# Performance work log

Hardware: AMD Instinct MI355X
Metric: run time of the kernel (lower is better)

The kernel has to match this reference:

```python
import jax, jax.numpy as jnp
import numpy as np
import math

B, QL, HID = 4, 4, 4096          # batch, speculative q_len, hidden_size
NH, NKV, HD = 32, 8, 128         # attention heads, kv heads, head_dim
GROUPS = NH // NKV               # GQA repeat factor = 4
PRIOR = 4096                     # cached (prior) KV length
THETA = 1.0e6                    # Mixtral rope_theta


def setup_inputs() -> dict:
    key = jax.random.key(0)
    ks = jax.random.split(key, 7)
    hidden_states = jax.random.normal(ks[0], (B, QL, HID), jnp.float32)
    past_k = jax.random.normal(ks[1], (B, NKV, PRIOR, HD), jnp.float32)
    past_v = jax.random.normal(ks[2], (B, NKV, PRIOR, HD), jnp.float32)
    wq = jax.random.normal(ks[3], (HID, NH * HD), jnp.float32) * 0.02
    wk = jax.random.normal(ks[4], (HID, NKV * HD), jnp.float32) * 0.02
    wv = jax.random.normal(ks[5], (HID, NKV * HD), jnp.float32) * 0.02
    wo = jax.random.normal(ks[6], (NH * HD, HID), jnp.float32) * 0.02
    # prior mask: all cached positions visible
    attention_mask = jnp.ones((B, 1, QL, PRIOR), dtype=bool)
    # active mask: causal over the speculative window
    active_mask = jnp.broadcast_to(jnp.tril(jnp.ones((QL, QL), dtype=bool)), (B, 1, QL, QL))
    position_ids = jnp.broadcast_to(PRIOR + jnp.arange(QL, dtype=jnp.int64), (B, QL))
    return {"hidden_states": hidden_states, "past_k": past_k, "past_v": past_v,
            "wq": wq, "wk": wk, "wv": wv, "wo": wo,
            "attention_mask": attention_mask, "active_mask": active_mask,
            "position_ids": position_ids}


def _rotate_half(x):
    x1, x2 = jnp.split(x, 2, axis=-1)
    return jnp.concatenate([-x2, x1], axis=-1)


def _rope_cos_sin(position_ids):
    inv_freq = 1.0 / (THETA ** (jnp.arange(0, HD, 2, dtype=jnp.float32) / HD))  # [HD/2]
    freqs = position_ids.astype(jnp.float32)[..., None] * inv_freq              # [B,QL,HD/2]
    emb = jnp.concatenate([freqs, freqs], axis=-1)                              # [B,QL,HD]
    return jnp.cos(emb)[:, None], jnp.sin(emb)[:, None]                          # [B,1,QL,HD]


def reference(hidden_states, past_k, past_v, wq, wk, wv, wo,
              attention_mask, active_mask, position_ids):
    # fused QKV projection (no bias in Mixtral)
    q = (hidden_states @ wq).reshape(B, QL, NH, HD).transpose(0, 2, 1, 3)   # [B,NH,QL,HD]
    k = (hidden_states @ wk).reshape(B, QL, NKV, HD).transpose(0, 2, 1, 3)  # [B,NKV,QL,HD]
    v = (hidden_states @ wv).reshape(B, QL, NKV, HD).transpose(0, 2, 1, 3)
    # RoPE on Q and active K
    cos, sin = _rope_cos_sin(position_ids)
    q = q * cos + _rotate_half(q) * sin
    k = k * cos + _rotate_half(k) * sin
    # GQA repeat_kv
    k_prior = jnp.repeat(past_k, GROUPS, axis=1)  # [B,NH,PRIOR,HD]
    v_prior = jnp.repeat(past_v, GROUPS, axis=1)
    k_active = jnp.repeat(k, GROUPS, axis=1)      # [B,NH,QL,HD]
    v_active = jnp.repeat(v, GROUPS, axis=1)
    scale = 1.0 / math.sqrt(HD)
    neg = jnp.finfo(jnp.float32).min
    prior_scores = jnp.einsum('bhqd,bhkd->bhqk', q, k_prior) * scale
    prior_scores = jnp.where(attention_mask, prior_scores, neg)
    active_scores = jnp.einsum('bhqd,bhkd->bhqk', q, k_active) * scale
    active_scores = jnp.where(active_mask, active_scores, neg)   # is_speculation=True
    # decomposed softmax: shared max and shared divisor across prior/active
    max_score = jnp.maximum(prior_scores.max(-1, keepdims=True),
                            active_scores.max(-1, keepdims=True))
    prior_exp = jnp.exp(prior_scores - max_score)
    active_exp = jnp.exp(active_scores - max_score)
    divisor = prior_exp.sum(-1, keepdims=True) + active_exp.sum(-1, keepdims=True)
    attn = (jnp.einsum('bhqk,bhkd->bhqd', prior_exp / divisor, v_prior) +
            jnp.einsum('bhqk,bhkd->bhqd', active_exp / divisor, v_active))
    attn = attn.transpose(0, 2, 1, 3).reshape(B, QL, NH * HD)
    return attn @ wo
```

## Files before the change

kernel.cpp:

```cpp
#include <hip/hip_runtime.h>
#include <math.h>

#define NROWS 16
#define NCOLS 6144
#define HID   4096
#define NKV   8
#define HD    128
#define PRIOR 4096
#define NCH   32
#define CHUNK 128
#define SUB   64
#define KC1   128
#define NKC   32

__device__ __forceinline__ float rdlane(float v, int l) {
    return __int_as_float(__builtin_amdgcn_readlane(__float_as_int(v), l));
}

__global__ __launch_bounds__(128)
void k_qkv_partial(const float* __restrict__ hid,
                   const float* __restrict__ wq,
                   const float* __restrict__ wk,
                   const float* __restrict__ wv,
                   float* __restrict__ part)
{
    const int t   = threadIdx.x;
    const int col = blockIdx.x * 256 + t * 2;
    const int kc  = blockIdx.y;
    const int k0  = kc * KC1;
    const float* w; int wn, wcol;
    if (col < 4096)      { w = wq; wn = 4096; wcol = col; }
    else if (col < 5120) { w = wk; wn = 1024; wcol = col - 4096; }
    else                 { w = wv; wn = 1024; wcol = col - 5120; }
    const float* wp = w + wcol + (size_t)k0 * wn;

    float acc[NROWS][2];
#pragma unroll
    for (int m = 0; m < NROWS; m++) { acc[m][0] = 0.f; acc[m][1] = 0.f; }
#pragma unroll 4
    for (int kk = 0; kk < KC1; kk += 4) {
        const float2 w0 = *(const float2*)(wp + (size_t)(kk + 0) * wn);
        const float2 w1 = *(const float2*)(wp + (size_t)(kk + 1) * wn);
        const float2 w2 = *(const float2*)(wp + (size_t)(kk + 2) * wn);
        const float2 w3 = *(const float2*)(wp + (size_t)(kk + 3) * wn);
#pragma unroll
        for (int m = 0; m < NROWS; m++) {
            const float4 h4 = *(const float4*)(hid + (size_t)m * HID + k0 + kk);
            acc[m][0] = fmaf(h4.x, w0.x, fmaf(h4.y, w1.x, fmaf(h4.z, w2.x, fmaf(h4.w, w3.x, acc[m][0]))));
            acc[m][1] = fmaf(h4.x, w0.y, fmaf(h4.y, w1.y, fmaf(h4.z, w2.y, fmaf(h4.w, w3.y, acc[m][1]))));
        }
    }
    float* po = part + (size_t)kc * (NROWS * NCOLS) + col;
#pragma unroll
    for (int m = 0; m < NROWS; m++)
        *(float2*)(po + (size_t)m * NCOLS) = make_float2(acc[m][0], acc[m][1]);
}

__global__ __launch_bounds__(256)
void k_reduce_rope(const float* __restrict__ part, float* __restrict__ qkv)
{
    const int tid = blockIdx.x * 256 + threadIdx.x;
    const double L64 = 0.21586735246819178;

    if (tid < 32768) {
        const int d = tid & 63, h = (tid >> 6) & 31, r = tid >> 11;
        const int c1 = h * HD + d;
        float s1 = 0.f, s2 = 0.f;
#pragma unroll 8
        for (int c = 0; c < NKC; c++) {
            const float* p = part + (size_t)c * (NROWS * NCOLS) + r * NCOLS + c1;
            s1 += p[0]; s2 += p[64];
        }
        const double ang = (double)(PRIOR + (r & 3)) * exp(-(double)d * L64);
        double sv, cv; sincos(ang, &sv, &cv);
        const float cf = (float)cv, sf = (float)sv, sc = 0.08838834764831845f;
        qkv[r * NCOLS + c1]      = (s1 * cf - s2 * sf) * sc;
        qkv[r * NCOLS + c1 + 64] = (s2 * cf + s1 * sf) * sc;
    } else if (tid < 40960) {
        const int idx = tid - 32768;
        const int d = idx & 63, kh = (idx >> 6) & 7, r = idx >> 9;
        const int c1 = 4096 + kh * HD + d;
        float s1 = 0.f, s2 = 0.f;
#pragma unroll 8
        for (int c = 0; c < NKC; c++) {
            const float* p = part + (size_t)c * (NROWS * NCOLS) + r * NCOLS + c1;
            s1 += p[0]; s2 += p[64];
        }
        const double ang = (double)(PRIOR + (r & 3)) * exp(-(double)d * L64);
        double sv, cv; sincos(ang, &sv, &cv);
        const float cf = (float)cv, sf = (float)sv;
        qkv[r * NCOLS + c1]      = s1 * cf - s2 * sf;
        qkv[r * NCOLS + c1 + 64] = s2 * cf + s1 * sf;
    } else {
        const int idx = tid - 40960;
        const int n = idx & 1023, r = idx >> 10;
        const int c1 = 5120 + n;
        float s = 0.f;
#pragma unroll 8
        for (int c = 0; c < NKC; c++)
            s += part[(size_t)c * (NROWS * NCOLS) + r * NCOLS + c1];
        qkv[r * NCOLS + c1] = s;
    }
}

__global__ __launch_bounds__(256, 4)
void k_attn_prior(const float* __restrict__ qkv,
                  const float* __restrict__ pk,
                  const float* __restrict__ pv,
                  float* __restrict__ part3)
{
    const int chunk = blockIdx.x, kvh = blockIdx.y, b = blockIdx.z;
    const int t = threadIdx.x;
    const int lane = t & 63;

    __shared__ float kT[128][64];
    __shared__ float qT[128][16];

    const int qt = t >> 6;
    const int h  = (lane >> 4) & 3;
    const int kt = lane & 15;

    const size_t kvoff = ((size_t)(b * NKV + kvh) * PRIOR + (size_t)chunk * CHUNK) * HD;
    const float* kbase = pk + kvoff;
    const float* vbase = pv + kvoff;

    float4 kreg[8];
    {
        const float* kr = kbase + (size_t)lane * HD + qt * 32;
#pragma unroll
        for (int i = 0; i < 8; i++) kreg[i] = *(const float4*)(kr + i * 4);
    }

    for (int i = t; i < 2048; i += 256) {
        const int r = i & 15, d = i >> 4;
        const int ql = r & 3, g = r >> 2;
        qT[d][r] = qkv[(size_t)(b * 4 + ql) * NCOLS + (kvh * 4 + g) * HD + d];
    }

    float m_r[4], l_r[4], o[4][2];
#pragma unroll
    for (int i = 0; i < 4; i++) { m_r[i] = -INFINITY; l_r[i] = 0.f; o[i][0] = 0.f; o[i][1] = 0.f; }

    for (int st = 0; st < CHUNK / SUB; st++) {
#pragma unroll
        for (int i = 0; i < 8; i++) {
            const int d = qt * 32 + i * 4;
            kT[d + 0][lane] = kreg[i].x; kT[d + 1][lane] = kreg[i].y;
            kT[d + 2][lane] = kreg[i].z; kT[d + 3][lane] = kreg[i].w;
        }
        if (st == 0) {
            const float* kr = kbase + (size_t)(SUB + lane) * HD + qt * 32;
#pragma unroll
            for (int i = 0; i < 8; i++) kreg[i] = *(const float4*)(kr + i * 4);
        }
        __syncthreads();

        float a[4][4];
#pragma unroll
        for (int i = 0; i < 4; i++)
#pragma unroll
            for (int j = 0; j < 4; j++) a[i][j] = 0.f;
#pragma unroll 4
        for (int dd = 0; dd < 32; dd++) {
            const int d = h * 32 + dd;
            const float4 q4 = *(const float4*)(&qT[d][qt * 4]);
            const float4 k4 = *(const float4*)(&kT[d][kt * 4]);
            a[0][0]=fmaf(q4.x,k4.x,a[0][0]); a[0][1]=fmaf(q4.x,k4.y,a[0][1]); a[0][2]=fmaf(q4.x,k4.z,a[0][2]); a[0][3]=fmaf(q4.x,k4.w,a[0][3]);
            a[1][0]=fmaf(q4.y,k4.x,a[1][0]); a[1][1]=fmaf(q4.y,k4.y,a[1][1]); a[1][2]=fmaf(q4.y,k4.z,a[1][2]); a[1][3]=fmaf(q4.y,k4.w,a[1][3]);
            a[2][0]=fmaf(q4.z,k4.x,a[2][0]); a[2][1]=fmaf(q4.z,k4.y,a[2][1]); a[2][2]=fmaf(q4.z,k4.z,a[2][2]); a[2][3]=fmaf(q4.z,k4.w,a[2][3]);
            a[3][0]=fmaf(q4.w,k4.x,a[3][0]); a[3][1]=fmaf(q4.w,k4.y,a[3][1]); a[3][2]=fmaf(q4.w,k4.z,a[3][2]); a[3][3]=fmaf(q4.w,k4.w,a[3][3]);
        }
        __syncthreads();

#pragma unroll
        for (int i = 0; i < 4; i++)
#pragma unroll
            for (int j = 0; j < 4; j++) {
                float v = a[i][j];
                v += __shfl_xor(v, 16);
                v += __shfl_xor(v, 32);
                a[i][j] = v;
            }
        float al[4], pr[4][4];
#pragma unroll
        for (int i = 0; i < 4; i++) {
            float mx = fmaxf(fmaxf(a[i][0], a[i][1]), fmaxf(a[i][2], a[i][3]));
            mx = fmaxf(mx, __shfl_xor(mx, 1));
            mx = fmaxf(mx, __shfl_xor(mx, 2));
            mx = fmaxf(mx, __shfl_xor(mx, 4));
            mx = fmaxf(mx, __shfl_xor(mx, 8));
            const float mn = fmaxf(m_r[i], mx);
            al[i] = __expf(m_r[i] - mn);
            m_r[i] = mn;
            float s = 0.f;
#pragma unroll
            for (int j = 0; j < 4; j++) { pr[i][j] = __expf(a[i][j] - mn); s += pr[i][j]; }
            s += __shfl_xor(s, 1); s += __shfl_xor(s, 2);
            s += __shfl_xor(s, 4); s += __shfl_xor(s, 8);
            l_r[i] = l_r[i] * al[i] + s;
        }
#pragma unroll
        for (int i = 0; i < 4; i++) { o[i][0] *= al[i]; o[i][1] *= al[i]; }

        const float* vs = vbase + (size_t)st * SUB * HD + (lane << 1);
#pragma unroll
        for (int g4 = 0; g4 < 16; g4++) {
            const float2 v0 = *(const float2*)(vs + (size_t)(g4 * 4 + 0) * HD);
            const float2 v1 = *(const float2*)(vs + (size_t)(g4 * 4 + 1) * HD);
            const float2 v2 = *(const float2*)(vs + (size_t)(g4 * 4 + 2) * HD);
            const float2 v3 = *(const float2*)(vs + (size_t)(g4 * 4 + 3) * HD);
#pragma unroll
            for (int i = 0; i < 4; i++) {
                const float p0 = rdlane(pr[i][0], g4);
                const float p1 = rdlane(pr[i][1], g4);
                const float p2 = rdlane(pr[i][2], g4);
                const float p3v = rdlane(pr[i][3], g4);
                o[i][0] = fmaf(p0,  v0.x, o[i][0]); o[i][1] = fmaf(p0,  v0.y, o[i][1]);
                o[i][0] = fmaf(p1,  v1.x, o[i][0]); o[i][1] = fmaf(p1,  v1.y, o[i][1]);
                o[i][0] = fmaf(p2,  v2.x, o[i][0]); o[i][1] = fmaf(p2,  v2.y, o[i][1]);
                o[i][0] = fmaf(p3v, v3.x, o[i][0]); o[i][1] = fmaf(p3v, v3.y, o[i][1]);
            }
        }
    }

    float* pout = part3 + (size_t)((b * NKV + kvh) * NCH + chunk) * 2080;
    if (lane == 0) {
#pragma unroll
        for (int i = 0; i < 4; i++) { pout[qt * 4 + i] = m_r[i]; pout[16 + qt * 4 + i] = l_r[i]; }
    }
#pragma unroll
    for (int i = 0; i < 4; i++)
        *(float2*)(pout + 32 + (size_t)(qt * 4 + i) * HD + (lane << 1)) =
            make_float2(o[i][0], o[i][1]);
}

__global__ __launch_bounds__(256)
void k_combine(const float* __restrict__ qkv,
               const float* __restrict__ part3,
               float* __restrict__ attn)
{
    const int g = blockIdx.x & 3, kvh = (blockIdx.x >> 2) & 7, b = blockIdx.x >> 5;
    const int t = threadIdx.x;
    __shared__ float qL[4][128], kA[4][128], vA[4][128];
    __shared__ float mC[NCH][4], lC[NCH][4], fC[NCH][4];
    __shared__ float sAct[4][4], pA[4][4], invL[4];

    for (int i = t; i < 512; i += 256) {
        const int ql = i >> 7, d = i & 127;
        qL[ql][d] = qkv[(size_t)(b * 4 + ql) * NCOLS + (kvh * 4 + g) * HD + d];
        kA[ql][d] = qkv[(size_t)(b * 4 + ql) * NCOLS + 4096 + kvh * HD + d];
        vA[ql][d] = qkv[(size_t)(b * 4 + ql) * NCOLS + 5120 + kvh * HD + d];
    }
    const float* p3 = part3 + (size_t)(b * NKV + kvh) * NCH * 2080;
    for (int i = t; i < NCH * 4; i += 256) {
        const int c = i >> 2, lr = i & 3;
        mC[c][lr] = p3[c * 2080 + g * 4 + lr];
        lC[c][lr] = p3[c * 2080 + 16 + g * 4 + lr];
    }
    __syncthreads();
    if (t < 128) {
        const int pp = t >> 3, dd = t & 7;
        const int lr = pp >> 2, k = pp & 3;
        float s = 0.f;
#pragma unroll
        for (int d = 0; d < 16; d++)
            s = fmaf(qL[lr][dd * 16 + d], kA[k][dd * 16 + d], s);
        s += __shfl_xor(s, 1); s += __shfl_xor(s, 2); s += __shfl_xor(s, 4);
        if (dd == 0) sAct[lr][k] = s;
    }
    __syncthreads();
    if (t < 128) {
        const int lr = t >> 5, c = t & 31;
        const float m  = mC[c][lr];
        const bool act = (c < 4) && (c <= lr);
        const float sa = act ? sAct[lr][c] : -INFINITY;
        float M = fmaxf(m, sa);
        M = fmaxf(M, __shfl_xor(M, 1));
        M = fmaxf(M, __shfl_xor(M, 2));
        M = fmaxf(M, __shfl_xor(M, 4));
        M = fmaxf(M, __shfl_xor(M, 8));
        M = fmaxf(M, __shfl_xor(M, 16));
        const float f = __expf(m - M);
        fC[c][lr] = f;
        const float pact = act ? __expf(sa - M) : 0.f;
        if (c < 4) pA[lr][c] = pact;
        float l = fmaf(f, lC[c][lr], pact);
        l += __shfl_xor(l, 1); l += __shfl_xor(l, 2);
        l += __shfl_xor(l, 4); l += __shfl_xor(l, 8); l += __shfl_xor(l, 16);
        if (c == 0) invL[lr] = 1.f / l;
    }
    __syncthreads();

    const int d = t & 127, hr = t >> 7;
    const int lr0 = hr * 2, lr1 = hr * 2 + 1;
    float o0 = 0.f, o1 = 0.f;
#pragma unroll 4
    for (int c = 0; c < NCH; c++) {
        const float f0 = fC[c][lr0], f1 = fC[c][lr1];
        const float* pa = p3 + c * 2080 + 32 + (g * 4 + lr0) * HD + d;
        o0 = fmaf(f0, pa[0],  o0);
        o1 = fmaf(f1, pa[HD], o1);
    }
#pragma unroll
    for (int k = 0; k < 4; k++) {
        const float v = vA[k][d];
        o0 = fmaf(pA[lr0][k], v, o0);
        o1 = fmaf(pA[lr1][k], v, o1);
    }
    attn[(size_t)(b * 4 + lr0) * HID + (kvh * 4 + g) * HD + d] = o0 * invL[lr0];
    attn[(size_t)(b * 4 + lr1) * HID + (kvh * 4 + g) * HD + d] = o1 * invL[lr1];
}

__global__ __launch_bounds__(128)
void k_out_partial(const float* __restrict__ attn,
                   const float* __restrict__ wo,
                   float* __restrict__ part)
{
    const int t = threadIdx.x;
    const int col = blockIdx.x * 256 + t * 2;
    const int kc = blockIdx.y;
    const int k0 = kc * KC1;
    const float* wp = wo + col + (size_t)k0 * HID;

    float acc[NROWS][2];
#pragma unroll
    for (int m = 0; m < NROWS; m++) { acc[m][0] = 0.f; acc[m][1] = 0.f; }
#pragma unroll 4
    for (int kk = 0; kk < KC1; kk += 4) {
        const float2 w0 = *(const float2*)(wp + (size_t)(kk + 0) * HID);
        const float2 w1 = *(const float2*)(wp + (size_t)(kk + 1) * HID);
        const float2 w2 = *(const float2*)(wp + (size_t)(kk + 2) * HID);
        const float2 w3 = *(const float2*)(wp + (size_t)(kk + 3) * HID);
#pragma unroll
        for (int m = 0; m < NROWS; m++) {
            const float4 h4 = *(const float4*)(attn + (size_t)m * HID + k0 + kk);
            acc[m][0] = fmaf(h4.x, w0.x, fmaf(h4.y, w1.x, fmaf(h4.z, w2.x, fmaf(h4.w, w3.x, acc[m][0]))));
            acc[m][1] = fmaf(h4.x, w0.y, fmaf(h4.y, w1.y, fmaf(h4.z, w2.y, fmaf(h4.w, w3.y, acc[m][1]))));
        }
    }
    float* po = part + (size_t)kc * (NROWS * HID) + col;
#pragma unroll
    for (int m = 0; m < NROWS; m++)
        *(float2*)(po + (size_t)m * HID) = make_float2(acc[m][0], acc[m][1]);
}

__global__ __launch_bounds__(256)
void k_out_reduce(const float* __restrict__ part, float* __restrict__ out)
{
    const int tid = blockIdx.x * 256 + threadIdx.x;
    const float* p = part + (size_t)tid * 4;
    float4 s = make_float4(0.f, 0.f, 0.f, 0.f);
#pragma unroll 8
    for (int c = 0; c < NKC; c++) {
        const float4 a = *(const float4*)(p + (size_t)c * (NROWS * HID));
        s.x += a.x; s.y += a.y; s.z += a.z; s.w += a.w;
    }
    *(float4*)(out + (size_t)tid * 4) = s;
}

extern "C" void kernel_launch(void* const* d_in, const int* in_sizes, int n_in,
                              void* d_out, int out_size, void* d_ws, size_t ws_size,
                              hipStream_t stream)
{
    (void)in_sizes; (void)n_in; (void)out_size; (void)ws_size;
    const float* hid = (const float*)d_in[0];
    const float* pk  = (const float*)d_in[1];
    const float* pv  = (const float*)d_in[2];
    const float* wq  = (const float*)d_in[3];
    const float* wk  = (const float*)d_in[4];
    const float* wv  = (const float*)d_in[5];
    const float* wo  = (const float*)d_in[6];
    float* out = (float*)d_out;
    float* ws  = (float*)d_ws;

    float* P1   = ws;
    float* P3   = ws;
    float* P5   = ws;
    float* qkv  = ws + 3145728;
    float* attn = ws + 3244032;

    k_qkv_partial<<<dim3(24, NKC), 128, 0, stream>>>(hid, wq, wk, wv, P1);
    k_reduce_rope<<<224, 256, 0, stream>>>(P1, qkv);
    k_attn_prior<<<dim3(NCH, NKV, 4), 256, 0, stream>>>(qkv, pk, pv, P3);
    k_combine<<<128, 256, 0, stream>>>(qkv, P3, attn);
    k_out_partial<<<dim3(16, NKC), 128, 0, stream>>>(attn, wo, P5);
    k_out_reduce<<<64, 256, 0, stream>>>(P5, out);
}
```

Before: 328.7 us.

## Double split-K chunks, parallelize reductions across lanes, prefetch V, split combine blocks

```diff
diff --git a/kernel.cpp b/kernel.cpp
--- a/kernel.cpp
+++ b/kernel.cpp
@@ -10,8 +10,10 @@
 #define NCH   32
 #define CHUNK 128
 #define SUB   64
-#define KC1   128
-#define NKC   32
+#define KCQ   64
+#define NKCQ  64
+#define KCO   64
+#define NKCO  64
 
 __device__ __forceinline__ float rdlane(float v, int l) {
     return __int_as_float(__builtin_amdgcn_readlane(__float_as_int(v), l));
@@ -27,7 +29,7 @@
     const int t   = threadIdx.x;
     const int col = blockIdx.x * 256 + t * 2;
     const int kc  = blockIdx.y;
-    const int k0  = kc * KC1;
+    const int k0  = kc * KCQ;
     const float* w; int wn, wcol;
     if (col < 4096)      { w = wq; wn = 4096; wcol = col; }
     else if (col < 5120) { w = wk; wn = 1024; wcol = col - 4096; }
@@ -38,7 +40,7 @@
 #pragma unroll
     for (int m = 0; m < NROWS; m++) { acc[m][0] = 0.f; acc[m][1] = 0.f; }
 #pragma unroll 4
-    for (int kk = 0; kk < KC1; kk += 4) {
+    for (int kk = 0; kk < KCQ; kk += 4) {
         const float2 w0 = *(const float2*)(wp + (size_t)(kk + 0) * wn);
         const float2 w1 = *(const float2*)(wp + (size_t)(kk + 1) * wn);
         const float2 w2 = *(const float2*)(wp + (size_t)(kk + 2) * wn);
@@ -59,47 +61,60 @@
 __global__ __launch_bounds__(256)
 void k_reduce_rope(const float* __restrict__ part, float* __restrict__ qkv)
 {
-    const int tid = blockIdx.x * 256 + threadIdx.x;
+    const int tid  = blockIdx.x * 256 + threadIdx.x;
+    const int w    = tid >> 6, lane = tid & 63;
+    const int u    = w * 16 + (lane & 15);
+    const int sub  = lane >> 4;
+    const int cs   = sub * 16;
     const double L64 = 0.21586735246819178;
 
-    if (tid < 32768) {
-        const int d = tid & 63, h = (tid >> 6) & 31, r = tid >> 11;
+    if (u < 32768) {
+        const int d = u & 63, h = (u >> 6) & 31, r = u >> 11;
         const int c1 = h * HD + d;
         float s1 = 0.f, s2 = 0.f;
 #pragma unroll 8
-        for (int c = 0; c < NKC; c++) {
-            const float* p = part + (size_t)c * (NROWS * NCOLS) + r * NCOLS + c1;
+        for (int i = 0; i < 16; i++) {
+            const float* p = part + (size_t)(cs + i) * (NROWS * NCOLS) + r * NCOLS + c1;
             s1 += p[0]; s2 += p[64];
         }
-        const double ang = (double)(PRIOR + (r & 3)) * exp(-(double)d * L64);
-        double sv, cv; sincos(ang, &sv, &cv);
-        const float cf = (float)cv, sf = (float)sv, sc = 0.08838834764831845f;
-        qkv[r * NCOLS + c1]      = (s1 * cf - s2 * sf) * sc;
-        qkv[r * NCOLS + c1 + 64] = (s2 * cf + s1 * sf) * sc;
-    } else if (tid < 40960) {
-        const int idx = tid - 32768;
+        s1 += __shfl_xor(s1, 16); s1 += __shfl_xor(s1, 32);
+        s2 += __shfl_xor(s2, 16); s2 += __shfl_xor(s2, 32);
+        if (sub == 0) {
+            const double ang = (double)(PRIOR + (r & 3)) * exp(-(double)d * L64);
+            double sv, cv; sincos(ang, &sv, &cv);
+            const float cf = (float)cv, sf = (float)sv, sc = 0.08838834764831845f;
+            qkv[r * NCOLS + c1]      = (s1 * cf - s2 * sf) * sc;
+            qkv[r * NCOLS + c1 + 64] = (s2 * cf + s1 * sf) * sc;
+        }
+    } else if (u < 40960) {
+        const int idx = u - 32768;
         const int d = idx & 63, kh = (idx >> 6) & 7, r = idx >> 9;
         const int c1 = 4096 + kh * HD + d;
         float s1 = 0.f, s2 = 0.f;
 #pragma unroll 8
-        for (int c = 0; c < NKC; c++) {
-            const float* p = part + (size_t)c * (NROWS * NCOLS) + r * NCOLS + c1;
+        for (int i = 0; i < 16; i++) {
+            const float* p = part + (size_t)(cs + i) * (NROWS * NCOLS) + r * NCOLS + c1;
             s1 += p[0]; s2 += p[64];
         }
-        const double ang = (double)(PRIOR + (r & 3)) * exp(-(double)d * L64);
-        double sv, cv; sincos(ang, &sv, &cv);
-        const float cf = (float)cv, sf = (float)sv;
-        qkv[r * NCOLS + c1]      = s1 * cf - s2 * sf;
-        qkv[r * NCOLS + c1 + 64] = s2 * cf + s1 * sf;
+        s1 += __shfl_xor(s1, 16); s1 += __shfl_xor(s1, 32);
+        s2 += __shfl_xor(s2, 16); s2 += __shfl_xor(s2, 32);
+        if (sub == 0) {
+            const double ang = (double)(PRIOR + (r & 3)) * exp(-(double)d * L64);
+            double sv, cv; sincos(ang, &sv, &cv);
+            const float cf = (float)cv, sf = (float)sv;
+            qkv[r * NCOLS + c1]      = s1 * cf - s2 * sf;
+            qkv[r * NCOLS + c1 + 64] = s2 * cf + s1 * sf;
+        }
     } else {
-        const int idx = tid - 40960;
+        const int idx = u - 40960;
         const int n = idx & 1023, r = idx >> 10;
         const int c1 = 5120 + n;
         float s = 0.f;
 #pragma unroll 8
-        for (int c = 0; c < NKC; c++)
-            s += part[(size_t)c * (NROWS * NCOLS) + r * NCOLS + c1];
-        qkv[r * NCOLS + c1] = s;
+        for (int i = 0; i < 16; i++)
+            s += part[(size_t)(cs + i) * (NROWS * NCOLS) + r * NCOLS + c1];
+        s += __shfl_xor(s, 16); s += __shfl_xor(s, 32);
+        if (sub == 0) qkv[r * NCOLS + c1] = s;
     }
 }
 
@@ -172,6 +187,14 @@
         }
         __syncthreads();
 
+        const float* vs = vbase + (size_t)st * SUB * HD + (lane << 1);
+        float2 vb[4][4];
+#pragma unroll
+        for (int g = 0; g < 4; ++g)
+#pragma unroll
+            for (int j = 0; j < 4; ++j)
+                vb[g][j] = *(const float2*)(vs + (size_t)(g * 4 + j) * HD);
+
 #pragma unroll
         for (int i = 0; i < 4; i++)
 #pragma unroll
@@ -202,13 +225,17 @@
 #pragma unroll
         for (int i = 0; i < 4; i++) { o[i][0] *= al[i]; o[i][1] *= al[i]; }
 
-        const float* vs = vbase + (size_t)st * SUB * HD + (lane << 1);
-#pragma unroll
-        for (int g4 = 0; g4 < 16; g4++) {
-            const float2 v0 = *(const float2*)(vs + (size_t)(g4 * 4 + 0) * HD);
-            const float2 v1 = *(const float2*)(vs + (size_t)(g4 * 4 + 1) * HD);
-            const float2 v2 = *(const float2*)(vs + (size_t)(g4 * 4 + 2) * HD);
-            const float2 v3 = *(const float2*)(vs + (size_t)(g4 * 4 + 3) * HD);
+#pragma unroll
+        for (int g4 = 0; g4 < 16; ++g4) {
+            const float2 v0 = vb[g4 & 3][0];
+            const float2 v1 = vb[g4 & 3][1];
+            const float2 v2 = vb[g4 & 3][2];
+            const float2 v3 = vb[g4 & 3][3];
+            if (g4 < 12) {
+#pragma unroll
+                for (int j = 0; j < 4; ++j)
+                    vb[g4 & 3][j] = *(const float2*)(vs + (size_t)((g4 + 4) * 4 + j) * HD);
+            }
 #pragma unroll
             for (int i = 0; i < 4; i++) {
                 const float p0 = rdlane(pr[i][0], g4);
@@ -234,46 +261,52 @@
             make_float2(o[i][0], o[i][1]);
 }
 
-__global__ __launch_bounds__(256)
+__global__ __launch_bounds__(128)
 void k_combine(const float* __restrict__ qkv,
                const float* __restrict__ part3,
                float* __restrict__ attn)
 {
-    const int g = blockIdx.x & 3, kvh = (blockIdx.x >> 2) & 7, b = blockIdx.x >> 5;
+    const int bid = blockIdx.x;
+    const int hr = bid & 1, g = (bid >> 1) & 3, kvh = (bid >> 3) & 7, b = bid >> 6;
     const int t = threadIdx.x;
-    __shared__ float qL[4][128], kA[4][128], vA[4][128];
-    __shared__ float mC[NCH][4], lC[NCH][4], fC[NCH][4];
-    __shared__ float sAct[4][4], pA[4][4], invL[4];
-
-    for (int i = t; i < 512; i += 256) {
+    const int lr0 = hr * 2, lr1 = lr0 + 1;
+    __shared__ float qL[2][128], kA[4][128], vA[4][128];
+    __shared__ float mC[NCH][2], lC[NCH][2], fC[NCH][2];
+    __shared__ float sAct[2][4], pA[2][4], invL[2];
+
+    for (int i = t; i < 256; i += 128) {
+        const int lrl = i >> 7, d = i & 127;
+        qL[lrl][d] = qkv[(size_t)(b * 4 + lr0 + lrl) * NCOLS + (kvh * 4 + g) * HD + d];
+    }
+    for (int i = t; i < 512; i += 128) {
         const int ql = i >> 7, d = i & 127;
-        qL[ql][d] = qkv[(size_t)(b * 4 + ql) * NCOLS + (kvh * 4 + g) * HD + d];
         kA[ql][d] = qkv[(size_t)(b * 4 + ql) * NCOLS + 4096 + kvh * HD + d];
         vA[ql][d] = qkv[(size_t)(b * 4 + ql) * NCOLS + 5120 + kvh * HD + d];
     }
     const float* p3 = part3 + (size_t)(b * NKV + kvh) * NCH * 2080;
-    for (int i = t; i < NCH * 4; i += 256) {
-        const int c = i >> 2, lr = i & 3;
-        mC[c][lr] = p3[c * 2080 + g * 4 + lr];
-        lC[c][lr] = p3[c * 2080 + 16 + g * 4 + lr];
+    for (int i = t; i < NCH * 2; i += 128) {
+        const int c = i >> 1, lrl = i & 1;
+        mC[c][lrl] = p3[c * 2080 + g * 4 + lr0 + lrl];
+        lC[c][lrl] = p3[c * 2080 + 16 + g * 4 + lr0 + lrl];
     }
     __syncthreads();
-    if (t < 128) {
+    if (t < 64) {
         const int pp = t >> 3, dd = t & 7;
-        const int lr = pp >> 2, k = pp & 3;
+        const int lrl = pp >> 2, k = pp & 3;
         float s = 0.f;
 #pragma unroll
         for (int d = 0; d < 16; d++)
-            s = fmaf(qL[lr][dd * 16 + d], kA[k][dd * 16 + d], s);
+            s = fmaf(qL[lrl][dd * 16 + d], kA[k][dd * 16 + d], s);
         s += __shfl_xor(s, 1); s += __shfl_xor(s, 2); s += __shfl_xor(s, 4);
-        if (dd == 0) sAct[lr][k] = s;
+        if (dd == 0) sAct[lrl][k] = s;
     }
     __syncthreads();
-    if (t < 128) {
-        const int lr = t >> 5, c = t & 31;
-        const float m  = mC[c][lr];
+    if (t < 64) {
+        const int lrl = t >> 5, c = t & 31;
+        const int lr = lr0 + lrl;
+        const float m  = mC[c][lrl];
         const bool act = (c < 4) && (c <= lr);
-        const float sa = act ? sAct[lr][c] : -INFINITY;
+        const float sa = act ? sAct[lrl][c] : -INFINITY;
         float M = fmaxf(m, sa);
         M = fmaxf(M, __shfl_xor(M, 1));
         M = fmaxf(M, __shfl_xor(M, 2));
@@ -281,34 +314,32 @@
         M = fmaxf(M, __shfl_xor(M, 8));
         M = fmaxf(M, __shfl_xor(M, 16));
         const float f = __expf(m - M);
-        fC[c][lr] = f;
+        fC[c][lrl] = f;
         const float pact = act ? __expf(sa - M) : 0.f;
-        if (c < 4) pA[lr][c] = pact;
-        float l = fmaf(f, lC[c][lr], pact);
+        if (c < 4) pA[lrl][c] = pact;
+        float l = fmaf(f, lC[c][lrl], pact);
         l += __shfl_xor(l, 1); l += __shfl_xor(l, 2);
         l += __shfl_xor(l, 4); l += __shfl_xor(l, 8); l += __shfl_xor(l, 16);
-        if (c == 0) invL[lr] = 1.f / l;
+        if (c == 0) invL[lrl] = 1.f / l;
     }
     __syncthreads();
 
-    const int d = t & 127, hr = t >> 7;
-    const int lr0 = hr * 2, lr1 = hr * 2 + 1;
+    const int d = t;
     float o0 = 0.f, o1 = 0.f;
 #pragma unroll 4
     for (int c = 0; c < NCH; c++) {
-        const float f0 = fC[c][lr0], f1 = fC[c][lr1];
         const float* pa = p3 + c * 2080 + 32 + (g * 4 + lr0) * HD + d;
-        o0 = fmaf(f0, pa[0],  o0);
-        o1 = fmaf(f1, pa[HD], o1);
+        o0 = fmaf(fC[c][0], pa[0],  o0);
+        o1 = fmaf(fC[c][1], pa[HD], o1);
     }
 #pragma unroll
     for (int k = 0; k < 4; k++) {
         const float v = vA[k][d];
-        o0 = fmaf(pA[lr0][k], v, o0);
-        o1 = fmaf(pA[lr1][k], v, o1);
-    }
-    attn[(size_t)(b * 4 + lr0) * HID + (kvh * 4 + g) * HD + d] = o0 * invL[lr0];
-    attn[(size_t)(b * 4 + lr1) * HID + (kvh * 4 + g) * HD + d] = o1 * invL[lr1];
+        o0 = fmaf(pA[0][k], v, o0);
+        o1 = fmaf(pA[1][k], v, o1);
+    }
+    attn[(size_t)(b * 4 + lr0) * HID + (kvh * 4 + g) * HD + d] = o0 * invL[0];
+    attn[(size_t)(b * 4 + lr1) * HID + (kvh * 4 + g) * HD + d] = o1 * invL[1];
 }
 
 __global__ __launch_bounds__(128)
@@ -319,14 +350,14 @@
     const int t = threadIdx.x;
     const int col = blockIdx.x * 256 + t * 2;
     const int kc = blockIdx.y;
-    const int k0 = kc * KC1;
+    const int k0 = kc * KCO;
     const float* wp = wo + col + (size_t)k0 * HID;
 
     float acc[NROWS][2];
 #pragma unroll
     for (int m = 0; m < NROWS; m++) { acc[m][0] = 0.f; acc[m][1] = 0.f; }
 #pragma unroll 4
-    for (int kk = 0; kk < KC1; kk += 4) {
+    for (int kk = 0; kk < KCO; kk += 4) {
         const float2 w0 = *(const float2*)(wp + (size_t)(kk + 0) * HID);
         const float2 w1 = *(const float2*)(wp + (size_t)(kk + 1) * HID);
         const float2 w2 = *(const float2*)(wp + (size_t)(kk + 2) * HID);
@@ -348,14 +379,21 @@
 void k_out_reduce(const float* __restrict__ part, float* __restrict__ out)
 {
     const int tid = blockIdx.x * 256 + threadIdx.x;
-    const float* p = part + (size_t)tid * 4;
+    const int w = tid >> 6, lane = tid & 63;
+    const int oid = w * 16 + (lane & 15);
+    const int sub = lane >> 4;
+    const float* p = part + (size_t)oid * 4 + (size_t)(sub * 16) * (NROWS * HID);
     float4 s = make_float4(0.f, 0.f, 0.f, 0.f);
 #pragma unroll 8
-    for (int c = 0; c < NKC; c++) {
+    for (int c = 0; c < 16; c++) {
         const float4 a = *(const float4*)(p + (size_t)c * (NROWS * HID));
         s.x += a.x; s.y += a.y; s.z += a.z; s.w += a.w;
     }
-    *(float4*)(out + (size_t)tid * 4) = s;
+    s.x += __shfl_xor(s.x, 16); s.x += __shfl_xor(s.x, 32);
+    s.y += __shfl_xor(s.y, 16); s.y += __shfl_xor(s.y, 32);
+    s.z += __shfl_xor(s.z, 16); s.z += __shfl_xor(s.z, 32);
+    s.w += __shfl_xor(s.w, 16); s.w += __shfl_xor(s.w, 32);
+    if (sub == 0) *(float4*)(out + (size_t)oid * 4) = s;
 }
 
 extern "C" void kernel_launch(void* const* d_in, const int* in_sizes, int n_in,
@@ -376,13 +414,13 @@
     float* P1   = ws;
     float* P3   = ws;
     float* P5   = ws;
-    float* qkv  = ws + 3145728;
-    float* attn = ws + 3244032;
-
-    k_qkv_partial<<<dim3(24, NKC), 128, 0, stream>>>(hid, wq, wk, wv, P1);
-    k_reduce_rope<<<224, 256, 0, stream>>>(P1, qkv);
+    float* qkv  = ws + 6291456;
+    float* attn = ws + 6389760;
+
+    k_qkv_partial<<<dim3(24, NKCQ), 128, 0, stream>>>(hid, wq, wk, wv, P1);
+    k_reduce_rope<<<896, 256, 0, stream>>>(P1, qkv);
     k_attn_prior<<<dim3(NCH, NKV, 4), 256, 0, stream>>>(qkv, pk, pv, P3);
-    k_combine<<<128, 256, 0, stream>>>(qkv, P3, attn);
-    k_out_partial<<<dim3(16, NKC), 128, 0, stream>>>(attn, wo, P5);
-    k_out_reduce<<<64, 256, 0, stream>>>(P5, out);
-}
+    k_combine<<<256, 128, 0, stream>>>(qkv, P3, attn);
+    k_out_partial<<<dim3(16, NKCO), 128, 0, stream>>>(attn, wo, P5);
+    k_out_reduce<<<256, 256, 0, stream>>>(P5, out);
+}
```

Result: faster. 314.9 us (-4.2%).
